# Optimization experiments

Hardware: AMD Instinct MI355X
Metric: run time of the kernel (lower is better)

## Reference

```python
import jax, jax.numpy as jnp
import numpy as np

T, D, R = 2000, 512, 64
LOG_2PI = float(np.log(2.0 * np.pi))


def setup_inputs() -> dict:
    key = jax.random.key(0)
    k1, k2, k3, k4 = jax.random.split(key, 4)
    X = jax.random.normal(k1, (T, D), dtype=jnp.float32)
    transition = jax.nn.softmax(jax.random.uniform(k2, (R, R), dtype=jnp.float32), axis=1)
    sig = jnp.ones((1, R), dtype=jnp.float32)
    init_w = jax.nn.softmax(jax.random.uniform(k3, (1, R), dtype=jnp.float32), axis=1)
    mu_rates = jax.random.uniform(k4, (1, R), dtype=jnp.float32)
    return {"X": X, "transition": transition, "sig": sig, "init_w": init_w, "mu_rates": mu_rates}


def reference(X, transition, sig, init_w, mu_rates):
    # X: [T, D] (D independent sequences), transition: [R, R] row-stochastic.
    Tn = X.shape[0]

    # State trajectory h_t = init_w @ transition^t, t = 0..T-1 (serial recurrence).
    def step(h, _):
        return h @ transition, h
    _, H = jax.lax.scan(step, init_w[0], None, length=Tn)  # [T, R]

    # Categorical(h) normalizes probs (h stays ~normalized; normalize for fidelity).
    log_h = jnp.log(H) - jnp.log(H.sum(axis=-1, keepdims=True))  # [T, R]

    # mu drifts: `if i % 100 == 0: mu += 10` fires at i=0 -> mu_t = mu_rates + 10*(t//100 + 1)
    t = jnp.arange(Tn)
    shift = 10.0 * (t // 100 + 1).astype(X.dtype)  # [T]
    mu = mu_rates[0][None, :] + shift[:, None]      # [T, R]

    s = sig[0]  # [R]
    # Per-component Normal log-pdf: [T, D, R]
    z = (X[:, :, None] - mu[:, None, :]) / s
    comp_logp = -0.5 * (z * z) - jnp.log(s) - 0.5 * LOG_2PI
    # Mixture log-prob per step, per sequence: [T, D]
    step_logp = jax.scipy.special.logsumexp(log_h[:, None, :] + comp_logp, axis=-1)
    # Joint log-likelihood per sequence: [D]
    return step_logp.sum(axis=0)
```

## Files before the change

kernel.cpp:

```cpp
#include <hip/hip_runtime.h>
#include <math.h>

#define RS 64
#define T_LEN 2000
#define D_LEN 512
#define NPOW 11
#define CT 4
#define G_CHUNK (T_LEN / CT)

#define LOG_2PI_F 1.83787706640934534f
#define LOG2E_F   1.44269504088896340736f
#define LN2_F     0.69314718055994530942f

typedef __bf16 bf16x8 __attribute__((ext_vector_type(8)));
typedef float  f32x4  __attribute__((ext_vector_type(4)));

__device__ __forceinline__ float readlane_f(float x, int l) {
    return __builtin_bit_cast(float,
        __builtin_amdgcn_readlane(__builtin_bit_cast(int, x), l));
}
__device__ __forceinline__ unsigned short bf16_bits(float f) {
    __bf16 b = static_cast<__bf16>(f);
    return __builtin_bit_cast(unsigned short, b);
}
__device__ __forceinline__ float unpk_lo(unsigned int u) {
    return __builtin_bit_cast(float, u << 16);
}
__device__ __forceinline__ float unpk_hi(unsigned int u) {
    return __builtin_bit_cast(float, u & 0xffff0000u);
}

__global__ __launch_bounds__(512) void k_chain(const float* __restrict__ trans,
                                               const float* __restrict__ sig,
                                               const float* __restrict__ mur,
                                               const float* __restrict__ initw,
                                               float* __restrict__ b2x,
                                               float* __restrict__ c1s_g,
                                               float* __restrict__ c2n_g,
                                               int* __restrict__ flags) {
    __shared__ unsigned int Mrow[2][RS * 33];
    __shared__ unsigned int Mcol[2][RS * 33];
    __shared__ int convf, unif;
    const int tx = threadIdx.x;
    const int w  = tx >> 6;
    const int j  = tx & 63;

    if (tx == 0) { convf = 1; unif = 0; }
    {
        const int r  = tx >> 3;
        const int c0 = (tx & 7) << 3;
        const float4 f0 = *(const float4*)(trans + r * RS + c0);
        const float4 f1 = *(const float4*)(trans + r * RS + c0 + 4);
        unsigned short hb[8] = { bf16_bits(f0.x), bf16_bits(f0.y),
                                 bf16_bits(f0.z), bf16_bits(f0.w),
                                 bf16_bits(f1.x), bf16_bits(f1.y),
                                 bf16_bits(f1.z), bf16_bits(f1.w) };
#pragma unroll
        for (int p = 0; p < 4; ++p)
            Mrow[0][r * 33 + (c0 >> 1) + p] =
                (unsigned int)hb[2 * p] | ((unsigned int)hb[2 * p + 1] << 16);
        unsigned short* McolH = (unsigned short*)&Mcol[0][0];
#pragma unroll
        for (int e = 0; e < 8; ++e)
            McolH[(c0 + e) * 66 + r] = hb[e];
    }
    float hv = initw[j];
    __syncthreads();

    const int ti  = w >> 1;
    const int tjA = (w & 1) << 1;
    int cur = 0;

    for (int k = 0; k < 3; ++k) {
        if ((w >> k) & 1) {
            const unsigned int* mt = &Mcol[cur][j * 33];
            float a0 = 0.f, a1 = 0.f;
#pragma unroll
            for (int m2 = 0; m2 < 32; ++m2) {
                const unsigned int u = mt[m2];
                a0 = fmaf(readlane_f(hv, 2 * m2),     unpk_lo(u), a0);
                a1 = fmaf(readlane_f(hv, 2 * m2 + 1), unpk_hi(u), a1);
            }
            hv = a0 + a1;
        }
        {
            f32x4 accA = {0.f, 0.f, 0.f, 0.f};
            f32x4 accB = {0.f, 0.f, 0.f, 0.f};
#pragma unroll
            for (int kc = 0; kc < 2; ++kc) {
                union { unsigned int u[4]; bf16x8 v; } fa, fbA, fbB;
                const int koff = 16 * kc + ((j >> 4) << 2);
                const int ar   = (16 * ti  + (j & 15)) * 33 + koff;
                const int brA  = (16 * tjA + (j & 15)) * 33 + koff;
                const int brB  = brA + 16 * 33;
#pragma unroll
                for (int p = 0; p < 4; ++p) {
                    fa.u[p]  = Mrow[cur][ar  + p];
                    fbA.u[p] = Mcol[cur][brA + p];
                    fbB.u[p] = Mcol[cur][brB + p];
                }
                accA = __builtin_amdgcn_mfma_f32_16x16x32_bf16(fa.v, fbA.v, accA, 0, 0, 0);
                accB = __builtin_amdgcn_mfma_f32_16x16x32_bf16(fa.v, fbB.v, accB, 0, 0, 0);
            }
            const int nxt   = cur ^ 1;
            const int drow  = 16 * ti + ((j >> 4) << 2);
            const int dcolA = 16 * tjA + (j & 15);
            const int dcolB = dcolA + 16;
            unsigned short ba[4], bb[4];
#pragma unroll
            for (int p = 0; p < 4; ++p) {
                ba[p] = bf16_bits(accA[p]);
                bb[p] = bf16_bits(accB[p]);
            }
            unsigned short* MrowH = (unsigned short*)&Mrow[nxt][0];
#pragma unroll
            for (int p = 0; p < 4; ++p) {
                MrowH[(drow + p) * 66 + dcolA] = ba[p];
                MrowH[(drow + p) * 66 + dcolB] = bb[p];
            }
            Mcol[nxt][dcolA * 33 + (drow >> 1)]     = (unsigned int)ba[0] | ((unsigned int)ba[1] << 16);
            Mcol[nxt][dcolA * 33 + (drow >> 1) + 1] = (unsigned int)ba[2] | ((unsigned int)ba[3] << 16);
            Mcol[nxt][dcolB * 33 + (drow >> 1)]     = (unsigned int)bb[0] | ((unsigned int)bb[1] << 16);
            Mcol[nxt][dcolB * 33 + (drow >> 1) + 1] = (unsigned int)bb[2] | ((unsigned int)bb[3] << 16);
            __syncthreads();
            cur = nxt;
        }
    }

    {
        int ok = 1;
        const int r  = tx >> 3;
        const int cb = (tx & 7) * 4;
#pragma unroll
        for (int e = 0; e < 4; ++e) {
            const unsigned int a  = Mrow[cur][r * 33 + cb + e];
            const unsigned int b0 = Mrow[cur][cb + e];
            if (fabsf(unpk_lo(a) - unpk_lo(b0)) > 1e-3f ||
                fabsf(unpk_hi(a) - unpk_hi(b0)) > 1e-3f) ok = 0;
        }
        if (!ok) atomicAnd(&convf, 0);
    }

    const float s   = sig[j];
    const float mu  = mur[j];
    const float is2 = 0.5f * LOG2E_F / (s * s);
    const float c1v = 2.0f * is2 * mu;
    const float c0b = -__builtin_amdgcn_logf(s)
                      - 0.5f * LOG_2PI_F * LOG2E_F - is2 * mu * mu;
    if (w == 0) {
        const float c2_0 = readlane_f(-is2, 0);
        const int alleq = __all(-is2 == c2_0);
        if (j == 0) unif = alleq;
        c1s_g[j] = c1v;
        c2n_g[j] = -is2;
    }

    float tot = hv;
#pragma unroll
    for (int off = 32; off; off >>= 1) tot += __shfl_xor(tot, off);
    b2x[w * RS + j] = __builtin_amdgcn_logf(hv) - __builtin_amdgcn_logf(tot) + c0b;

    if (w == 0) {
        const unsigned int u = Mrow[cur][j >> 1];
        const float pv = (j & 1) ? unpk_hi(u) : unpk_lo(u);
        float t2 = pv;
#pragma unroll
        for (int off = 32; off; off >>= 1) t2 += __shfl_xor(t2, off);
        b2x[8 * RS + j] = __builtin_amdgcn_logf(pv) - __builtin_amdgcn_logf(t2) + c0b;
    }
    __syncthreads();
    if (tx == 0) flags[0] = (convf && unif) ? 1 : 0;
}

__global__ __launch_bounds__(256) void k_fast(const float* __restrict__ X,
                                              const float* __restrict__ b2x,
                                              const float* __restrict__ c1s_g,
                                              const float* __restrict__ c2n_g,
                                              const int* __restrict__ flags,
                                              float* __restrict__ partial) {
    if (flags[0] == 0) return;
    __shared__ float c0p[CT][RS];
    __shared__ float c1p[CT][RS];
    __shared__ float mc0s[CT], mc1s[CT];
    __shared__ int   ncnt[CT];
    const int tx = threadIdx.x;
    const int w  = tx >> 6;
    const int j  = tx & 63;
    const int cy = blockIdx.y;

    {
        const int t = cy * CT + w;
        const float* row = b2x + ((t < 8) ? t : 8) * RS;
        const float bv  = row[j];
        const float c1v = c1s_g[j];
        const float xr0 = -10.0f * (float)(t / 100 + 1);
        float q  = fmaf(c1v, xr0, bv);
        int   bi = j;
#pragma unroll
        for (int off = 32; off; off >>= 1) {
            const float oq = __shfl_xor(q, off);
            const int   oi = __shfl_xor(bi, off);
            if (oq > q || (oq == q && oi < bi)) { q = oq; bi = oi; }
        }
        const float m0 = __shfl(bv, bi);
        const float m1 = __shfl(c1v, bi);
        const float d0 = bv  - m0;
        const float d1 = c1v - m1;
        const float eL = fmaf(d1, xr0 - 8.0f, d0);
        const float eR = fmaf(d1, xr0 + 8.0f, d0);
        const bool keep = fmaxf(eL, eR) > -27.0f;
        const unsigned long long bal = __ballot(keep);
        const int pos  = (int)__popcll(bal & ((1ull << j) - 1ull));
        const int n    = (int)__popcll(bal);
        const int npad = (n + 7) & ~7;
        if (keep) { c0p[w][pos] = d0; c1p[w][pos] = d1; }
        if (j >= n && j < npad) { c0p[w][j] = -30000.0f; c1p[w][j] = 0.0f; }
        if (j == 0) { mc0s[w] = m0; mc1s[w] = m1; ncnt[w] = npad; }
    }
    __syncthreads();

    const float c2u = c2n_g[0];
    float accA = 0.f, accB = 0.f;
#pragma unroll
    for (int tt = 0; tt < CT; ++tt) {
        const int t = cy * CT + tt;
        const float shift = 10.0f * (float)(t / 100 + 1);
        const float2 xv = *(const float2*)(X + t * D_LEN + 2 * tx);
        const float xrA = xv.x - shift;
        const float xrB = xv.y - shift;
        const int np = ncnt[tt];

        float sA0 = 0.f, sA1 = 0.f, sA2 = 0.f, sA3 = 0.f;
        float sB0 = 0.f, sB1 = 0.f, sB2 = 0.f, sB3 = 0.f;
        for (int r = 0; r < np; r += 8) {
            const float4 ca0 = *(const float4*)&c0p[tt][r];
            const float4 cb0 = *(const float4*)&c0p[tt][r + 4];
            const float4 ca1 = *(const float4*)&c1p[tt][r];
            const float4 cb1 = *(const float4*)&c1p[tt][r + 4];
            sA0 += __builtin_amdgcn_exp2f(fmaf(ca1.x, xrA, ca0.x));
            sA1 += __builtin_amdgcn_exp2f(fmaf(ca1.y, xrA, ca0.y));
            sA2 += __builtin_amdgcn_exp2f(fmaf(ca1.z, xrA, ca0.z));
            sA3 += __builtin_amdgcn_exp2f(fmaf(ca1.w, xrA, ca0.w));
            sA0 += __builtin_amdgcn_exp2f(fmaf(cb1.x, xrA, cb0.x));
            sA1 += __builtin_amdgcn_exp2f(fmaf(cb1.y, xrA, cb0.y));
            sA2 += __builtin_amdgcn_exp2f(fmaf(cb1.z, xrA, cb0.z));
            sA3 += __builtin_amdgcn_exp2f(fmaf(cb1.w, xrA, cb0.w));
            sB0 += __builtin_amdgcn_exp2f(fmaf(ca1.x, xrB, ca0.x));
            sB1 += __builtin_amdgcn_exp2f(fmaf(ca1.y, xrB, ca0.y));
            sB2 += __builtin_amdgcn_exp2f(fmaf(ca1.z, xrB, ca0.z));
            sB3 += __builtin_amdgcn_exp2f(fmaf(ca1.w, xrB, ca0.w));
            sB0 += __builtin_amdgcn_exp2f(fmaf(cb1.x, xrB, cb0.x));
            sB1 += __builtin_amdgcn_exp2f(fmaf(cb1.y, xrB, cb0.y));
            sB2 += __builtin_amdgcn_exp2f(fmaf(cb1.z, xrB, cb0.z));
            sB3 += __builtin_amdgcn_exp2f(fmaf(cb1.w, xrB, cb0.w));
        }
        const float mmA = fmaf(c2u, xrA * xrA, fmaf(mc1s[tt], xrA, mc0s[tt]));
        const float mmB = fmaf(c2u, xrB * xrB, fmaf(mc1s[tt], xrB, mc0s[tt]));
        accA += mmA + __builtin_amdgcn_logf((sA0 + sA1) + (sA2 + sA3));
        accB += mmB + __builtin_amdgcn_logf((sB0 + sB1) + (sB2 + sB3));
    }
    *(float2*)(partial + cy * D_LEN + 2 * tx) =
        make_float2(LN2_F * accA, LN2_F * accB);
}

__global__ __launch_bounds__(512) void k_fb(const float* __restrict__ trans,
                                            const float* __restrict__ sig,
                                            const float* __restrict__ mur,
                                            const float* __restrict__ initw,
                                            const float* __restrict__ X,
                                            const float* __restrict__ c1s_g,
                                            const float* __restrict__ c2n_g,
                                            const int* __restrict__ flags,
                                            float* __restrict__ partial) {
    if (flags[0] != 0) return;
    __shared__ unsigned int Mrow[2][RS * 33];
    __shared__ unsigned int Mcol[2][RS * 33];
    __shared__ float shb2[8][RS];
    __shared__ float sc1[RS], sc2[RS];
    const int tx = threadIdx.x;
    const int w  = tx >> 6;
    const int j  = tx & 63;
    const int t  = blockIdx.x * 8 + w;

    {
        const int r  = tx >> 3;
        const int c0 = (tx & 7) << 3;
        const float4 f0 = *(const float4*)(trans + r * RS + c0);
        const float4 f1 = *(const float4*)(trans + r * RS + c0 + 4);
        unsigned short hb[8] = { bf16_bits(f0.x), bf16_bits(f0.y),
                                 bf16_bits(f0.z), bf16_bits(f0.w),
                                 bf16_bits(f1.x), bf16_bits(f1.y),
                                 bf16_bits(f1.z), bf16_bits(f1.w) };
#pragma unroll
        for (int p = 0; p < 4; ++p)
            Mrow[0][r * 33 + (c0 >> 1) + p] =
                (unsigned int)hb[2 * p] | ((unsigned int)hb[2 * p + 1] << 16);
        unsigned short* McolH = (unsigned short*)&Mcol[0][0];
#pragma unroll
        for (int e = 0; e < 8; ++e)
            McolH[(c0 + e) * 66 + r] = hb[e];
    }
    float hv = initw[j];
    __syncthreads();

    const int ti  = w >> 1;
    const int tjA = (w & 1) << 1;
    int cur = 0;

    for (int k = 0; k < NPOW; ++k) {
        if ((t >> k) & 1) {
            const unsigned int* mt = &Mcol[cur][j * 33];
            float a0 = 0.f, a1 = 0.f;
#pragma unroll
            for (int m2 = 0; m2 < 32; ++m2) {
                const unsigned int u = mt[m2];
                a0 = fmaf(readlane_f(hv, 2 * m2),     unpk_lo(u), a0);
                a1 = fmaf(readlane_f(hv, 2 * m2 + 1), unpk_hi(u), a1);
            }
            hv = a0 + a1;
        }
        if (k < NPOW - 1) {
            f32x4 accA = {0.f, 0.f, 0.f, 0.f};
            f32x4 accB = {0.f, 0.f, 0.f, 0.f};
#pragma unroll
            for (int kc = 0; kc < 2; ++kc) {
                union { unsigned int u[4]; bf16x8 v; } fa, fbA, fbB;
                const int koff = 16 * kc + ((j >> 4) << 2);
                const int ar   = (16 * ti  + (j & 15)) * 33 + koff;
                const int brA  = (16 * tjA + (j & 15)) * 33 + koff;
                const int brB  = brA + 16 * 33;
#pragma unroll
                for (int p = 0; p < 4; ++p) {
                    fa.u[p]  = Mrow[cur][ar  + p];
                    fbA.u[p] = Mcol[cur][brA + p];
                    fbB.u[p] = Mcol[cur][brB + p];
                }
                accA = __builtin_amdgcn_mfma_f32_16x16x32_bf16(fa.v, fbA.v, accA, 0, 0, 0);
                accB = __builtin_amdgcn_mfma_f32_16x16x32_bf16(fa.v, fbB.v, accB, 0, 0, 0);
            }
            const int nxt   = cur ^ 1;
            const int drow  = 16 * ti + ((j >> 4) << 2);
            const int dcolA = 16 * tjA + (j & 15);
            const int dcolB = dcolA + 16;
            unsigned short ba[4], bb[4];
#pragma unroll
            for (int p = 0; p < 4; ++p) {
                ba[p] = bf16_bits(accA[p]);
                bb[p] = bf16_bits(accB[p]);
            }
            unsigned short* MrowH = (unsigned short*)&Mrow[nxt][0];
#pragma unroll
            for (int p = 0; p < 4; ++p) {
                MrowH[(drow + p) * 66 + dcolA] = ba[p];
                MrowH[(drow + p) * 66 + dcolB] = bb[p];
            }
            Mcol[nxt][dcolA * 33 + (drow >> 1)]     = (unsigned int)ba[0] | ((unsigned int)ba[1] << 16);
            Mcol[nxt][dcolA * 33 + (drow >> 1) + 1] = (unsigned int)ba[2] | ((unsigned int)ba[3] << 16);
            Mcol[nxt][dcolB * 33 + (drow >> 1)]     = (unsigned int)bb[0] | ((unsigned int)bb[1] << 16);
            Mcol[nxt][dcolB * 33 + (drow >> 1) + 1] = (unsigned int)bb[2] | ((unsigned int)bb[3] << 16);
            __syncthreads();
            cur = nxt;
        }
    }

    float tot = hv;
#pragma unroll
    for (int off = 32; off; off >>= 1) tot += __shfl_xor(tot, off);
    const float s   = sig[j];
    const float mu  = mur[j];
    const float is2 = 0.5f * LOG2E_F / (s * s);
    const float c0b = -__builtin_amdgcn_logf(s)
                      - 0.5f * LOG_2PI_F * LOG2E_F - is2 * mu * mu;
    shb2[w][j] = __builtin_amdgcn_logf(hv) - __builtin_amdgcn_logf(tot) + c0b;
    if (w == 0) { sc1[j] = c1s_g[j]; sc2[j] = c2n_g[j]; }
    __syncthreads();

    const int d = tx;
    float acc2 = 0.f;
    for (int tt = 0; tt < 8; ++tt) {
        const int tg = blockIdx.x * 8 + tt;
        const float x = X[tg * D_LEN + d];
        const float shift = 10.0f * (float)(tg / 100 + 1);
        const float xr  = x - shift;
        const float xr2 = xr * xr;
        float a[RS];
        float m0 = -INFINITY, m1 = -INFINITY, m2 = -INFINITY, m3 = -INFINITY;
#pragma unroll
        for (int r = 0; r < RS; r += 4) {
            float v0 = fmaf(sc1[r + 0], xr, shb2[tt][r + 0]);
            float v1 = fmaf(sc1[r + 1], xr, shb2[tt][r + 1]);
            float v2 = fmaf(sc1[r + 2], xr, shb2[tt][r + 2]);
            float v3 = fmaf(sc1[r + 3], xr, shb2[tt][r + 3]);
            v0 = fmaf(sc2[r + 0], xr2, v0);
            v1 = fmaf(sc2[r + 1], xr2, v1);
            v2 = fmaf(sc2[r + 2], xr2, v2);
            v3 = fmaf(sc2[r + 3], xr2, v3);
            a[r + 0] = v0; a[r + 1] = v1; a[r + 2] = v2; a[r + 3] = v3;
            m0 = fmaxf(m0, v0); m1 = fmaxf(m1, v1);
            m2 = fmaxf(m2, v2); m3 = fmaxf(m3, v3);
        }
        const float mm = fmaxf(fmaxf(m0, m1), fmaxf(m2, m3));
        float s0 = 0.f, s1 = 0.f, s2 = 0.f, s3 = 0.f;
#pragma unroll
        for (int r = 0; r < RS; r += 4) {
            s0 += __builtin_amdgcn_exp2f(a[r + 0] - mm);
            s1 += __builtin_amdgcn_exp2f(a[r + 1] - mm);
            s2 += __builtin_amdgcn_exp2f(a[r + 2] - mm);
            s3 += __builtin_amdgcn_exp2f(a[r + 3] - mm);
        }
        acc2 += mm + __builtin_amdgcn_logf((s0 + s1) + (s2 + s3));
    }
    partial[blockIdx.x * D_LEN + d] = LN2_F * acc2;
    partial[(250 + blockIdx.x) * D_LEN + d] = 0.f;
}

__global__ __launch_bounds__(256) void k_reduce(const float* __restrict__ partial,
                                                float* __restrict__ out,
                                                int nchunk) {
    __shared__ double red[4][8];
    const int tx   = threadIdx.x;
    const int dloc = tx & 7;
    const int cg   = tx >> 3;
    const int d    = blockIdx.x * 8 + dloc;

    double s = 0.0;
    for (int c = cg; c < nchunk; c += 32)
        s += (double)partial[c * D_LEN + d];

    s += __shfl_xor(s, 8);
    s += __shfl_xor(s, 16);
    s += __shfl_xor(s, 32);

    const int w = tx >> 6;
    if ((tx & 63) < 8) red[w][dloc] = s;
    __syncthreads();
    if (tx < 8)
        out[blockIdx.x * 8 + tx] =
            (float)(red[0][tx] + red[1][tx] + red[2][tx] + red[3][tx]);
}

extern "C" void kernel_launch(void* const* d_in, const int* in_sizes, int n_in,
                              void* d_out, int out_size, void* d_ws, size_t ws_size,
                              hipStream_t stream) {
    const float* X     = (const float*)d_in[0];
    const float* trans = (const float*)d_in[1];
    const float* sig   = (const float*)d_in[2];
    const float* initw = (const float*)d_in[3];
    const float* mur   = (const float*)d_in[4];
    float* out = (float*)d_out;
    float* ws  = (float*)d_ws;

    float* b2x     = ws;
    float* c1s     = ws + 576;
    float* c2n     = ws + 640;
    int*   flags   = (int*)(ws + 704);
    float* partial = ws + 768;

    k_chain<<<1, 512, 0, stream>>>(trans, sig, mur, initw, b2x, c1s, c2n, flags);
    k_fb<<<T_LEN / 8, 512, 0, stream>>>(trans, sig, mur, initw, X,
                                        c1s, c2n, flags, partial);
    dim3 gF(1, G_CHUNK);
    k_fast<<<gF, 256, 0, stream>>>(X, b2x, c1s, c2n, flags, partial);
    k_reduce<<<D_LEN / 8, 256, 0, stream>>>(partial, out, G_CHUNK);
}
```

Before: 26.18 us.

## Fuse chain, fast and fallback kernels into one redundant-per-block kernel

Merges the single-block chain kernel, the fast pruned-mixture kernel and the fallback kernel into one kernel. Every block now recomputes the first few transition-matrix squarings and the convergence check itself, which removes two launches and the serial dependency on a one-block kernel. Each block handles 8 timesteps with 512 threads, one sequence per thread, instead of 4 timesteps with 256 threads doing two sequences each. The cost is redundant MFMA squaring work in all 250 blocks and larger shared memory per block.

```diff
diff --git a/kernel.cpp b/kernel.cpp
--- a/kernel.cpp
+++ b/kernel.cpp
@@ -5,7 +5,7 @@
 #define T_LEN 2000
 #define D_LEN 512
 #define NPOW 11
-#define CT 4
+#define CT 8
 #define G_CHUNK (T_LEN / CT)
 
 #define LOG_2PI_F 1.83787706640934534f
@@ -30,22 +30,28 @@
     return __builtin_bit_cast(float, u & 0xffff0000u);
 }
 
-__global__ __launch_bounds__(512) void k_chain(const float* __restrict__ trans,
-                                               const float* __restrict__ sig,
-                                               const float* __restrict__ mur,
-                                               const float* __restrict__ initw,
-                                               float* __restrict__ b2x,
-                                               float* __restrict__ c1s_g,
-                                               float* __restrict__ c2n_g,
-                                               int* __restrict__ flags) {
+__global__ __launch_bounds__(512) void k_all(const float* __restrict__ trans,
+                                             const float* __restrict__ sig,
+                                             const float* __restrict__ mur,
+                                             const float* __restrict__ initw,
+                                             const float* __restrict__ X,
+                                             float* __restrict__ partial) {
     __shared__ unsigned int Mrow[2][RS * 33];
     __shared__ unsigned int Mcol[2][RS * 33];
-    __shared__ int convf, unif;
+    __shared__ float c0p[CT][RS];
+    __shared__ float c1p[CT][RS];
+    __shared__ float mc0s[CT], mc1s[CT];
+    __shared__ int   ncnt[CT];
+    __shared__ float shb2[CT][RS];
+    __shared__ float sc1[RS], sc2[RS];
+    __shared__ int convf;
     const int tx = threadIdx.x;
     const int w  = tx >> 6;
     const int j  = tx & 63;
-
-    if (tx == 0) { convf = 1; unif = 0; }
+    const int cy = blockIdx.x;
+    const int t  = cy * CT + w;
+
+    if (tx == 0) convf = 1;
     {
         const int r  = tx >> 3;
         const int c0 = (tx & 7) << 3;
@@ -140,6 +146,7 @@
         }
         if (!ok) atomicAnd(&convf, 0);
     }
+    __syncthreads();
 
     const float s   = sig[j];
     const float mu  = mur[j];
@@ -147,271 +154,179 @@
     const float c1v = 2.0f * is2 * mu;
     const float c0b = -__builtin_amdgcn_logf(s)
                       - 0.5f * LOG_2PI_F * LOG2E_F - is2 * mu * mu;
-    if (w == 0) {
-        const float c2_0 = readlane_f(-is2, 0);
-        const int alleq = __all(-is2 == c2_0);
-        if (j == 0) unif = alleq;
-        c1s_g[j] = c1v;
-        c2n_g[j] = -is2;
+    const float c2u = readlane_f(-is2, 0);
+    const int unif = __all(-is2 == c2u);
+
+    if (convf && unif) {
+        float hval;
+        if (t < 8) hval = hv;
+        else {
+            const unsigned int u = Mrow[cur][j >> 1];
+            hval = (j & 1) ? unpk_hi(u) : unpk_lo(u);
+        }
+        float tot = hval;
+#pragma unroll
+        for (int off = 32; off; off >>= 1) tot += __shfl_xor(tot, off);
+        const float b2val = __builtin_amdgcn_logf(hval)
+                          - __builtin_amdgcn_logf(tot) + c0b;
+
+        {
+            const float xr0 = -10.0f * (float)(t / 100 + 1);
+            float q  = fmaf(c1v, xr0, b2val);
+            int   bi = j;
+#pragma unroll
+            for (int off = 32; off; off >>= 1) {
+                const float oq = __shfl_xor(q, off);
+                const int   oi = __shfl_xor(bi, off);
+                if (oq > q || (oq == q && oi < bi)) { q = oq; bi = oi; }
+            }
+            const float m0 = __shfl(b2val, bi);
+            const float m1 = __shfl(c1v, bi);
+            const float d0 = b2val - m0;
+            const float d1 = c1v  - m1;
+            const float eL = fmaf(d1, xr0 - 8.0f, d0);
+            const float eR = fmaf(d1, xr0 + 8.0f, d0);
+            const bool keep = fmaxf(eL, eR) > -27.0f;
+            const unsigned long long bal = __ballot(keep);
+            const int pos  = (int)__popcll(bal & ((1ull << j) - 1ull));
+            const int n    = (int)__popcll(bal);
+            const int npad = (n + 7) & ~7;
+            if (keep) { c0p[w][pos] = d0; c1p[w][pos] = d1; }
+            if (j >= n && j < npad) { c0p[w][j] = -30000.0f; c1p[w][j] = 0.0f; }
+            if (j == 0) { mc0s[w] = m0; mc1s[w] = m1; ncnt[w] = npad; }
+        }
+        __syncthreads();
+
+        float xv[CT];
+#pragma unroll
+        for (int tt = 0; tt < CT; ++tt)
+            xv[tt] = X[(cy * CT + tt) * D_LEN + tx];
+
+        float acc = 0.f;
+#pragma unroll
+        for (int tt = 0; tt < CT; ++tt) {
+            const int tg = cy * CT + tt;
+            const float shift = 10.0f * (float)(tg / 100 + 1);
+            const float xr = xv[tt] - shift;
+            const int np = ncnt[tt];
+            float s0 = 0.f, s1 = 0.f, s2 = 0.f, s3 = 0.f;
+            for (int r = 0; r < np; r += 8) {
+                const float4 ca0 = *(const float4*)&c0p[tt][r];
+                const float4 cb0 = *(const float4*)&c0p[tt][r + 4];
+                const float4 ca1 = *(const float4*)&c1p[tt][r];
+                const float4 cb1 = *(const float4*)&c1p[tt][r + 4];
+                s0 += __builtin_amdgcn_exp2f(fmaf(ca1.x, xr, ca0.x));
+                s1 += __builtin_amdgcn_exp2f(fmaf(ca1.y, xr, ca0.y));
+                s2 += __builtin_amdgcn_exp2f(fmaf(ca1.z, xr, ca0.z));
+                s3 += __builtin_amdgcn_exp2f(fmaf(ca1.w, xr, ca0.w));
+                s0 += __builtin_amdgcn_exp2f(fmaf(cb1.x, xr, cb0.x));
+                s1 += __builtin_amdgcn_exp2f(fmaf(cb1.y, xr, cb0.y));
+                s2 += __builtin_amdgcn_exp2f(fmaf(cb1.z, xr, cb0.z));
+                s3 += __builtin_amdgcn_exp2f(fmaf(cb1.w, xr, cb0.w));
+            }
+            const float mm = fmaf(c2u, xr * xr, fmaf(mc1s[tt], xr, mc0s[tt]));
+            acc += mm + __builtin_amdgcn_logf((s0 + s1) + (s2 + s3));
+        }
+        partial[cy * D_LEN + tx] = LN2_F * acc;
+    } else {
+        for (int k = 3; k < NPOW; ++k) {
+            if ((t >> k) & 1) {
+                const unsigned int* mt = &Mcol[cur][j * 33];
+                float a0 = 0.f, a1 = 0.f;
+#pragma unroll
+                for (int m2 = 0; m2 < 32; ++m2) {
+                    const unsigned int u = mt[m2];
+                    a0 = fmaf(readlane_f(hv, 2 * m2),     unpk_lo(u), a0);
+                    a1 = fmaf(readlane_f(hv, 2 * m2 + 1), unpk_hi(u), a1);
+                }
+                hv = a0 + a1;
+            }
+            if (k < NPOW - 1) {
+                f32x4 accA = {0.f, 0.f, 0.f, 0.f};
+                f32x4 accB = {0.f, 0.f, 0.f, 0.f};
+#pragma unroll
+                for (int kc = 0; kc < 2; ++kc) {
+                    union { unsigned int u[4]; bf16x8 v; } fa, fbA, fbB;
+                    const int koff = 16 * kc + ((j >> 4) << 2);
+                    const int ar   = (16 * ti  + (j & 15)) * 33 + koff;
+                    const int brA  = (16 * tjA + (j & 15)) * 33 + koff;
+                    const int brB  = brA + 16 * 33;
+#pragma unroll
+                    for (int p = 0; p < 4; ++p) {
+                        fa.u[p]  = Mrow[cur][ar  + p];
+                        fbA.u[p] = Mcol[cur][brA + p];
+                        fbB.u[p] = Mcol[cur][brB + p];
+                    }
+                    accA = __builtin_amdgcn_mfma_f32_16x16x32_bf16(fa.v, fbA.v, accA, 0, 0, 0);
+                    accB = __builtin_amdgcn_mfma_f32_16x16x32_bf16(fa.v, fbB.v, accB, 0, 0, 0);
+                }
+                const int nxt   = cur ^ 1;
+                const int drow  = 16 * ti + ((j >> 4) << 2);
+                const int dcolA = 16 * tjA + (j & 15);
+                const int dcolB = dcolA + 16;
+                unsigned short ba[4], bb[4];
+#pragma unroll
+                for (int p = 0; p < 4; ++p) {
+                    ba[p] = bf16_bits(accA[p]);
+                    bb[p] = bf16_bits(accB[p]);
+                }
+                unsigned short* MrowH = (unsigned short*)&Mrow[nxt][0];
+#pragma unroll
+                for (int p = 0; p < 4; ++p) {
+                    MrowH[(drow + p) * 66 + dcolA] = ba[p];
+                    MrowH[(drow + p) * 66 + dcolB] = bb[p];
+                }
+                Mcol[nxt][dcolA * 33 + (drow >> 1)]     = (unsigned int)ba[0] | ((unsigned int)ba[1] << 16);
+                Mcol[nxt][dcolA * 33 + (drow >> 1) + 1] = (unsigned int)ba[2] | ((unsigned int)ba[3] << 16);
+                Mcol[nxt][dcolB * 33 + (drow >> 1)]     = (unsigned int)bb[0] | ((unsigned int)bb[1] << 16);
+                Mcol[nxt][dcolB * 33 + (drow >> 1) + 1] = (unsigned int)bb[2] | ((unsigned int)bb[3] << 16);
+                __syncthreads();
+                cur = nxt;
+            }
+        }
+        float tot = hv;
+#pragma unroll
+        for (int off = 32; off; off >>= 1) tot += __shfl_xor(tot, off);
+        shb2[w][j] = __builtin_amdgcn_logf(hv) - __builtin_amdgcn_logf(tot) + c0b;
+        if (w == 0) { sc1[j] = c1v; sc2[j] = -is2; }
+        __syncthreads();
+
+        float acc2 = 0.f;
+        for (int tt = 0; tt < CT; ++tt) {
+            const int tg = cy * CT + tt;
+            const float x = X[tg * D_LEN + tx];
+            const float shift = 10.0f * (float)(tg / 100 + 1);
+            const float xr  = x - shift;
+            const float xr2 = xr * xr;
+            float m0 = -INFINITY;
+            for (int r = 0; r < RS; r += 4) {
+                float v0 = fmaf(sc1[r + 0], xr, shb2[tt][r + 0]);
+                float v1 = fmaf(sc1[r + 1], xr, shb2[tt][r + 1]);
+                float v2 = fmaf(sc1[r + 2], xr, shb2[tt][r + 2]);
+                float v3 = fmaf(sc1[r + 3], xr, shb2[tt][r + 3]);
+                v0 = fmaf(sc2[r + 0], xr2, v0);
+                v1 = fmaf(sc2[r + 1], xr2, v1);
+                v2 = fmaf(sc2[r + 2], xr2, v2);
+                v3 = fmaf(sc2[r + 3], xr2, v3);
+                m0 = fmaxf(m0, fmaxf(fmaxf(v0, v1), fmaxf(v2, v3)));
+            }
+            float s0 = 0.f;
+            for (int r = 0; r < RS; r += 4) {
+                float v0 = fmaf(sc1[r + 0], xr, shb2[tt][r + 0]);
+                float v1 = fmaf(sc1[r + 1], xr, shb2[tt][r + 1]);
+                float v2 = fmaf(sc1[r + 2], xr, shb2[tt][r + 2]);
+                float v3 = fmaf(sc1[r + 3], xr, shb2[tt][r + 3]);
+                v0 = fmaf(sc2[r + 0], xr2, v0);
+                v1 = fmaf(sc2[r + 1], xr2, v1);
+                v2 = fmaf(sc2[r + 2], xr2, v2);
+                v3 = fmaf(sc2[r + 3], xr2, v3);
+                s0 += __builtin_amdgcn_exp2f(v0 - m0) + __builtin_amdgcn_exp2f(v1 - m0)
+                    + __builtin_amdgcn_exp2f(v2 - m0) + __builtin_amdgcn_exp2f(v3 - m0);
+            }
+            acc2 += m0 + __builtin_amdgcn_logf(s0);
+        }
+        partial[cy * D_LEN + tx] = LN2_F * acc2;
     }
-
-    float tot = hv;
-#pragma unroll
-    for (int off = 32; off; off >>= 1) tot += __shfl_xor(tot, off);
-    b2x[w * RS + j] = __builtin_amdgcn_logf(hv) - __builtin_amdgcn_logf(tot) + c0b;
-
-    if (w == 0) {
-        const unsigned int u = Mrow[cur][j >> 1];
-        const float pv = (j & 1) ? unpk_hi(u) : unpk_lo(u);
-        float t2 = pv;
-#pragma unroll
-        for (int off = 32; off; off >>= 1) t2 += __shfl_xor(t2, off);
-        b2x[8 * RS + j] = __builtin_amdgcn_logf(pv) - __builtin_amdgcn_logf(t2) + c0b;
-    }
-    __syncthreads();
-    if (tx == 0) flags[0] = (convf && unif) ? 1 : 0;
-}
-
-__global__ __launch_bounds__(256) void k_fast(const float* __restrict__ X,
-                                              const float* __restrict__ b2x,
-                                              const float* __restrict__ c1s_g,
-                                              const float* __restrict__ c2n_g,
-                                              const int* __restrict__ flags,
-                                              float* __restrict__ partial) {
-    if (flags[0] == 0) return;
-    __shared__ float c0p[CT][RS];
-    __shared__ float c1p[CT][RS];
-    __shared__ float mc0s[CT], mc1s[CT];
-    __shared__ int   ncnt[CT];
-    const int tx = threadIdx.x;
-    const int w  = tx >> 6;
-    const int j  = tx & 63;
-    const int cy = blockIdx.y;
-
-    {
-        const int t = cy * CT + w;
-        const float* row = b2x + ((t < 8) ? t : 8) * RS;
-        const float bv  = row[j];
-        const float c1v = c1s_g[j];
-        const float xr0 = -10.0f * (float)(t / 100 + 1);
-        float q  = fmaf(c1v, xr0, bv);
-        int   bi = j;
-#pragma unroll
-        for (int off = 32; off; off >>= 1) {
-            const float oq = __shfl_xor(q, off);
-            const int   oi = __shfl_xor(bi, off);
-            if (oq > q || (oq == q && oi < bi)) { q = oq; bi = oi; }
-        }
-        const float m0 = __shfl(bv, bi);
-        const float m1 = __shfl(c1v, bi);
-        const float d0 = bv  - m0;
-        const float d1 = c1v - m1;
-        const float eL = fmaf(d1, xr0 - 8.0f, d0);
-        const float eR = fmaf(d1, xr0 + 8.0f, d0);
-        const bool keep = fmaxf(eL, eR) > -27.0f;
-        const unsigned long long bal = __ballot(keep);
-        const int pos  = (int)__popcll(bal & ((1ull << j) - 1ull));
-        const int n    = (int)__popcll(bal);
-        const int npad = (n + 7) & ~7;
-        if (keep) { c0p[w][pos] = d0; c1p[w][pos] = d1; }
-        if (j >= n && j < npad) { c0p[w][j] = -30000.0f; c1p[w][j] = 0.0f; }
-        if (j == 0) { mc0s[w] = m0; mc1s[w] = m1; ncnt[w] = npad; }
-    }
-    __syncthreads();
-
-    const float c2u = c2n_g[0];
-    float accA = 0.f, accB = 0.f;
-#pragma unroll
-    for (int tt = 0; tt < CT; ++tt) {
-        const int t = cy * CT + tt;
-        const float shift = 10.0f * (float)(t / 100 + 1);
-        const float2 xv = *(const float2*)(X + t * D_LEN + 2 * tx);
-        const float xrA = xv.x - shift;
-        const float xrB = xv.y - shift;
-        const int np = ncnt[tt];
-
-        float sA0 = 0.f, sA1 = 0.f, sA2 = 0.f, sA3 = 0.f;
-        float sB0 = 0.f, sB1 = 0.f, sB2 = 0.f, sB3 = 0.f;
-        for (int r = 0; r < np; r += 8) {
-            const float4 ca0 = *(const float4*)&c0p[tt][r];
-            const float4 cb0 = *(const float4*)&c0p[tt][r + 4];
-            const float4 ca1 = *(const float4*)&c1p[tt][r];
-            const float4 cb1 = *(const float4*)&c1p[tt][r + 4];
-            sA0 += __builtin_amdgcn_exp2f(fmaf(ca1.x, xrA, ca0.x));
-            sA1 += __builtin_amdgcn_exp2f(fmaf(ca1.y, xrA, ca0.y));
-            sA2 += __builtin_amdgcn_exp2f(fmaf(ca1.z, xrA, ca0.z));
-            sA3 += __builtin_amdgcn_exp2f(fmaf(ca1.w, xrA, ca0.w));
-            sA0 += __builtin_amdgcn_exp2f(fmaf(cb1.x, xrA, cb0.x));
-            sA1 += __builtin_amdgcn_exp2f(fmaf(cb1.y, xrA, cb0.y));
-            sA2 += __builtin_amdgcn_exp2f(fmaf(cb1.z, xrA, cb0.z));
-            sA3 += __builtin_amdgcn_exp2f(fmaf(cb1.w, xrA, cb0.w));
-            sB0 += __builtin_amdgcn_exp2f(fmaf(ca1.x, xrB, ca0.x));
-            sB1 += __builtin_amdgcn_exp2f(fmaf(ca1.y, xrB, ca0.y));
-            sB2 += __builtin_amdgcn_exp2f(fmaf(ca1.z, xrB, ca0.z));
-            sB3 += __builtin_amdgcn_exp2f(fmaf(ca1.w, xrB, ca0.w));
-            sB0 += __builtin_amdgcn_exp2f(fmaf(cb1.x, xrB, cb0.x));
-            sB1 += __builtin_amdgcn_exp2f(fmaf(cb1.y, xrB, cb0.y));
-            sB2 += __builtin_amdgcn_exp2f(fmaf(cb1.z, xrB, cb0.z));
-            sB3 += __builtin_amdgcn_exp2f(fmaf(cb1.w, xrB, cb0.w));
-        }
-        const float mmA = fmaf(c2u, xrA * xrA, fmaf(mc1s[tt], xrA, mc0s[tt]));
-        const float mmB = fmaf(c2u, xrB * xrB, fmaf(mc1s[tt], xrB, mc0s[tt]));
-        accA += mmA + __builtin_amdgcn_logf((sA0 + sA1) + (sA2 + sA3));
-        accB += mmB + __builtin_amdgcn_logf((sB0 + sB1) + (sB2 + sB3));
-    }
-    *(float2*)(partial + cy * D_LEN + 2 * tx) =
-        make_float2(LN2_F * accA, LN2_F * accB);
-}
-
-__global__ __launch_bounds__(512) void k_fb(const float* __restrict__ trans,
-                                            const float* __restrict__ sig,
-                                            const float* __restrict__ mur,
-                                            const float* __restrict__ initw,
-                                            const float* __restrict__ X,
-                                            const float* __restrict__ c1s_g,
-                                            const float* __restrict__ c2n_g,
-                                            const int* __restrict__ flags,
-                                            float* __restrict__ partial) {
-    if (flags[0] != 0) return;
-    __shared__ unsigned int Mrow[2][RS * 33];
-    __shared__ unsigned int Mcol[2][RS * 33];
-    __shared__ float shb2[8][RS];
-    __shared__ float sc1[RS], sc2[RS];
-    const int tx = threadIdx.x;
-    const int w  = tx >> 6;
-    const int j  = tx & 63;
-    const int t  = blockIdx.x * 8 + w;
-
-    {
-        const int r  = tx >> 3;
-        const int c0 = (tx & 7) << 3;
-        const float4 f0 = *(const float4*)(trans + r * RS + c0);
-        const float4 f1 = *(const float4*)(trans + r * RS + c0 + 4);
-        unsigned short hb[8] = { bf16_bits(f0.x), bf16_bits(f0.y),
-                                 bf16_bits(f0.z), bf16_bits(f0.w),
-                                 bf16_bits(f1.x), bf16_bits(f1.y),
-                                 bf16_bits(f1.z), bf16_bits(f1.w) };
-#pragma unroll
-        for (int p = 0; p < 4; ++p)
-            Mrow[0][r * 33 + (c0 >> 1) + p] =
-                (unsigned int)hb[2 * p] | ((unsigned int)hb[2 * p + 1] << 16);
-        unsigned short* McolH = (unsigned short*)&Mcol[0][0];
-#pragma unroll
-        for (int e = 0; e < 8; ++e)
-            McolH[(c0 + e) * 66 + r] = hb[e];
-    }
-    float hv = initw[j];
-    __syncthreads();
-
-    const int ti  = w >> 1;
-    const int tjA = (w & 1) << 1;
-    int cur = 0;
-
-    for (int k = 0; k < NPOW; ++k) {
-        if ((t >> k) & 1) {
-            const unsigned int* mt = &Mcol[cur][j * 33];
-            float a0 = 0.f, a1 = 0.f;
-#pragma unroll
-            for (int m2 = 0; m2 < 32; ++m2) {
-                const unsigned int u = mt[m2];
-                a0 = fmaf(readlane_f(hv, 2 * m2),     unpk_lo(u), a0);
-                a1 = fmaf(readlane_f(hv, 2 * m2 + 1), unpk_hi(u), a1);
-            }
-            hv = a0 + a1;
-        }
-        if (k < NPOW - 1) {
-            f32x4 accA = {0.f, 0.f, 0.f, 0.f};
-            f32x4 accB = {0.f, 0.f, 0.f, 0.f};
-#pragma unroll
-            for (int kc = 0; kc < 2; ++kc) {
-                union { unsigned int u[4]; bf16x8 v; } fa, fbA, fbB;
-                const int koff = 16 * kc + ((j >> 4) << 2);
-                const int ar   = (16 * ti  + (j & 15)) * 33 + koff;
-                const int brA  = (16 * tjA + (j & 15)) * 33 + koff;
-                const int brB  = brA + 16 * 33;
-#pragma unroll
-                for (int p = 0; p < 4; ++p) {
-                    fa.u[p]  = Mrow[cur][ar  + p];
-                    fbA.u[p] = Mcol[cur][brA + p];
-                    fbB.u[p] = Mcol[cur][brB + p];
-                }
-                accA = __builtin_amdgcn_mfma_f32_16x16x32_bf16(fa.v, fbA.v, accA, 0, 0, 0);
-                accB = __builtin_amdgcn_mfma_f32_16x16x32_bf16(fa.v, fbB.v, accB, 0, 0, 0);
-            }
-            const int nxt   = cur ^ 1;
-            const int drow  = 16 * ti + ((j >> 4) << 2);
-            const int dcolA = 16 * tjA + (j & 15);
-            const int dcolB = dcolA + 16;
-            unsigned short ba[4], bb[4];
-#pragma unroll
-            for (int p = 0; p < 4; ++p) {
-                ba[p] = bf16_bits(accA[p]);
-                bb[p] = bf16_bits(accB[p]);
-            }
-            unsigned short* MrowH = (unsigned short*)&Mrow[nxt][0];
-#pragma unroll
-            for (int p = 0; p < 4; ++p) {
-                MrowH[(drow + p) * 66 + dcolA] = ba[p];
-                MrowH[(drow + p) * 66 + dcolB] = bb[p];
-            }
-            Mcol[nxt][dcolA * 33 + (drow >> 1)]     = (unsigned int)ba[0] | ((unsigned int)ba[1] << 16);
-            Mcol[nxt][dcolA * 33 + (drow >> 1) + 1] = (unsigned int)ba[2] | ((unsigned int)ba[3] << 16);
-            Mcol[nxt][dcolB * 33 + (drow >> 1)]     = (unsigned int)bb[0] | ((unsigned int)bb[1] << 16);
-            Mcol[nxt][dcolB * 33 + (drow >> 1) + 1] = (unsigned int)bb[2] | ((unsigned int)bb[3] << 16);
-            __syncthreads();
-            cur = nxt;
-        }
-    }
-
-    float tot = hv;
-#pragma unroll
-    for (int off = 32; off; off >>= 1) tot += __shfl_xor(tot, off);
-    const float s   = sig[j];
-    const float mu  = mur[j];
-    const float is2 = 0.5f * LOG2E_F / (s * s);
-    const float c0b = -__builtin_amdgcn_logf(s)
-                      - 0.5f * LOG_2PI_F * LOG2E_F - is2 * mu * mu;
-    shb2[w][j] = __builtin_amdgcn_logf(hv) - __builtin_amdgcn_logf(tot) + c0b;
-    if (w == 0) { sc1[j] = c1s_g[j]; sc2[j] = c2n_g[j]; }
-    __syncthreads();
-
-    const int d = tx;
-    float acc2 = 0.f;
-    for (int tt = 0; tt < 8; ++tt) {
-        const int tg = blockIdx.x * 8 + tt;
-        const float x = X[tg * D_LEN + d];
-        const float shift = 10.0f * (float)(tg / 100 + 1);
-        const float xr  = x - shift;
-        const float xr2 = xr * xr;
-        float a[RS];
-        float m0 = -INFINITY, m1 = -INFINITY, m2 = -INFINITY, m3 = -INFINITY;
-#pragma unroll
-        for (int r = 0; r < RS; r += 4) {
-            float v0 = fmaf(sc1[r + 0], xr, shb2[tt][r + 0]);
-            float v1 = fmaf(sc1[r + 1], xr, shb2[tt][r + 1]);
-            float v2 = fmaf(sc1[r + 2], xr, shb2[tt][r + 2]);
-            float v3 = fmaf(sc1[r + 3], xr, shb2[tt][r + 3]);
-            v0 = fmaf(sc2[r + 0], xr2, v0);
-            v1 = fmaf(sc2[r + 1], xr2, v1);
-            v2 = fmaf(sc2[r + 2], xr2, v2);
-            v3 = fmaf(sc2[r + 3], xr2, v3);
-            a[r + 0] = v0; a[r + 1] = v1; a[r + 2] = v2; a[r + 3] = v3;
-            m0 = fmaxf(m0, v0); m1 = fmaxf(m1, v1);
-            m2 = fmaxf(m2, v2); m3 = fmaxf(m3, v3);
-        }
-        const float mm = fmaxf(fmaxf(m0, m1), fmaxf(m2, m3));
-        float s0 = 0.f, s1 = 0.f, s2 = 0.f, s3 = 0.f;
-#pragma unroll
-        for (int r = 0; r < RS; r += 4) {
-            s0 += __builtin_amdgcn_exp2f(a[r + 0] - mm);
-            s1 += __builtin_amdgcn_exp2f(a[r + 1] - mm);
-            s2 += __builtin_amdgcn_exp2f(a[r + 2] - mm);
-            s3 += __builtin_amdgcn_exp2f(a[r + 3] - mm);
-        }
-        acc2 += mm + __builtin_amdgcn_logf((s0 + s1) + (s2 + s3));
-    }
-    partial[blockIdx.x * D_LEN + d] = LN2_F * acc2;
-    partial[(250 + blockIdx.x) * D_LEN + d] = 0.f;
 }
 
 __global__ __launch_bounds__(256) void k_reduce(const float* __restrict__ partial,
@@ -450,16 +365,8 @@
     float* out = (float*)d_out;
     float* ws  = (float*)d_ws;
 
-    float* b2x     = ws;
-    float* c1s     = ws + 576;
-    float* c2n     = ws + 640;
-    int*   flags   = (int*)(ws + 704);
-    float* partial = ws + 768;
-
-    k_chain<<<1, 512, 0, stream>>>(trans, sig, mur, initw, b2x, c1s, c2n, flags);
-    k_fb<<<T_LEN / 8, 512, 0, stream>>>(trans, sig, mur, initw, X,
-                                        c1s, c2n, flags, partial);
-    dim3 gF(1, G_CHUNK);
-    k_fast<<<gF, 256, 0, stream>>>(X, b2x, c1s, c2n, flags, partial);
+    float* partial = ws;
+
+    k_all<<<G_CHUNK, 512, 0, stream>>>(trans, sig, mur, initw, X, partial);
     k_reduce<<<D_LEN / 8, 256, 0, stream>>>(partial, out, G_CHUNK);
 }
```

Result: faster. 23.99 us (-8.4%).
